# Optimization experiments

Hardware: AMD Instinct MI355X
Metric: run time of the kernel (lower is better)

Reference implementation:

```python
import jax, jax.numpy as jnp
import numpy as np

N_NODES = 50000
N_EDGES = 600000
IN_FEATS = 128
N_HIDDEN = 128
N_CLASSES = 40


def setup_inputs() -> dict:
    key = jax.random.key(0)
    ks = jax.random.split(key, 12)
    feat = jax.random.normal(ks[0], (N_NODES, IN_FEATS), dtype=jnp.float32)
    src = jax.random.randint(ks[1], (N_EDGES,), 0, N_NODES, dtype=jnp.int32)
    dst = jax.random.randint(ks[2], (N_EDGES,), 0, N_NODES, dtype=jnp.int32)
    dims = [(IN_FEATS, N_HIDDEN), (N_HIDDEN, N_HIDDEN), (N_HIDDEN, N_CLASSES)]
    params = {}
    for i, (di, do) in enumerate(dims):
        s = 1.0 / np.sqrt(di)
        params[f"w_self{i}"] = jax.random.uniform(ks[3 + 3 * i], (di, do), jnp.float32, -s, s)
        params[f"w_neigh{i}"] = jax.random.uniform(ks[4 + 3 * i], (di, do), jnp.float32, -s, s)
        params[f"b{i}"] = jnp.zeros((do,), jnp.float32)
    return dict(feat=feat, src=src, dst=dst, **params)


def _sage_layer(h, src, dst, w_self, w_neigh, b):
    # mean aggregation over in-neighbors: msg = h[src], reduce at dst
    msg_sum = jax.ops.segment_sum(h[src], dst, num_segments=N_NODES)  # [N, d]
    deg = jax.ops.segment_sum(jnp.ones((src.shape[0],), h.dtype), dst, num_segments=N_NODES)
    h_neigh = msg_sum / jnp.maximum(deg, 1.0)[:, None]
    # DGL SAGEConv(mean): out = fc_self(h) + fc_neigh(mean_neigh) + bias
    return h @ w_self + h_neigh @ w_neigh + b


def reference(feat, src, dst,
              w_self0, w_neigh0, b0,
              w_self1, w_neigh1, b1,
              w_self2, w_neigh2, b2):
    # dropout p=0.0 -> identity
    h = _sage_layer(feat, src, dst, w_self0, w_neigh0, b0)
    h = jax.nn.relu(h)
    h = _sage_layer(h, src, dst, w_self1, w_neigh1, b1)
    h = jax.nn.relu(h)
    h = _sage_layer(h, src, dst, w_self2, w_neigh2, b2)
    return h
```

## Files before the change

kernel.cpp:

```cpp
#include <hip/hip_runtime.h>

#define N_NODES 50000
#define N_EDGES 600000

typedef short bf16x8 __attribute__((ext_vector_type(8)));
typedef float f32x4  __attribute__((ext_vector_type(4)));
typedef unsigned short u16x8 __attribute__((ext_vector_type(8)));
typedef unsigned short u16x4 __attribute__((ext_vector_type(4)));

__device__ inline ushort rne_bf16(float a) {
    union { float f; unsigned u; } v; v.f = a;
    return (ushort)((v.u + 0x7FFFu + ((v.u >> 16) & 1u)) >> 16);
}
__device__ inline float bf16_to_f32(ushort h) {
    return __uint_as_float((unsigned)h << 16);
}
__device__ inline void split_bf16(float a, ushort& hi, ushort& lo) {
    hi = rne_bf16(a);
    float hv = bf16_to_f32(hi);
    lo = rne_bf16(a - hv);
}


__global__ void count_deg_kernel(const int* __restrict__ dst, int* __restrict__ deg, int ne) {
    int e = blockIdx.x * blockDim.x + threadIdx.x;
    if (e < ne) atomicAdd(&deg[dst[e]], 1);
}

__global__ __launch_bounds__(256) void block_sums_kernel(const int* __restrict__ deg,
                                                         int* __restrict__ bsum, int n) {
    __shared__ int s[256];
    int t = threadIdx.x;
    int i = blockIdx.x * 256 + t;
    s[t] = (i < n) ? deg[i] : 0;
    __syncthreads();
    #pragma unroll
    for (int d = 128; d > 0; d >>= 1) {
        if (t < d) s[t] += s[t + d];
        __syncthreads();
    }
    if (t == 0) bsum[blockIdx.x] = s[0];
}

__global__ __launch_bounds__(256) void scan_bsums_kernel(const int* __restrict__ bsum,
                                                         int* __restrict__ base, int nb,
                                                         int* __restrict__ off, int n) {
    __shared__ int s[256];
    int t = threadIdx.x;
    int v = (t < nb) ? bsum[t] : 0;
    s[t] = v;
    __syncthreads();
    #pragma unroll
    for (int d = 1; d < 256; d <<= 1) {
        int x = (t >= d) ? s[t - d] : 0;
        __syncthreads();
        s[t] += x;
        __syncthreads();
    }
    if (t < nb) base[t] = s[t] - v;
    if (t == 255) off[n] = s[255];
}

__global__ __launch_bounds__(256) void scatter_offsets_kernel(const int* __restrict__ deg,
                                                              const int* __restrict__ base,
                                                              int* __restrict__ off,
                                                              int* __restrict__ cur, int n) {
    __shared__ int s[256];
    int t = threadIdx.x;
    int i = blockIdx.x * 256 + t;
    int v = (i < n) ? deg[i] : 0;
    s[t] = v;
    __syncthreads();
    #pragma unroll
    for (int d = 1; d < 256; d <<= 1) {
        int x = (t >= d) ? s[t - d] : 0;
        __syncthreads();
        s[t] += x;
        __syncthreads();
    }
    if (i < n) {
        int excl = s[t] - v + base[blockIdx.x];
        off[i] = excl;
        cur[i] = excl;
    }
}

__global__ void fill_csr_kernel(const int* __restrict__ src, const int* __restrict__ dst,
                                int* __restrict__ cur, int* __restrict__ ssrc, int ne) {
    int e = blockIdx.x * blockDim.x + threadIdx.x;
    if (e < ne) {
        int p = atomicAdd(&cur[dst[e]], 1);
        ssrc[p] = src[e];
    }
}

__global__ void convert_w_kernel(const float* __restrict__ Ws, const float* __restrict__ Wn,
                                 int dout, ushort* __restrict__ Bth, ushort* __restrict__ Btl) {
    int n = blockIdx.x;
    int k = threadIdx.x;
    float w = (n < dout) ? Ws[(long)k * dout + n] : Wn[(long)k * dout + (n - dout)];
    ushort hi, lo;
    split_bf16(w, hi, lo);
    Bth[n * 128 + k] = hi;
    Btl[n * 128 + k] = lo;
}


#define KDIM 128
#define APAD 136

__device__ inline void stage_a_full(const float* __restrict__ A, int bm, int M, int tid,
                                    ushort* __restrict__ Ahi, ushort* __restrict__ Alo) {
    const int m  = tid >> 2;
    const int kq = (tid & 3) * 32;
    const int grow = bm + m;
    #pragma unroll
    for (int g = 0; g < 4; ++g) {
        float f[8];
        if (grow < M) {
            const float* ap = A + (long)grow * KDIM + kq + g * 8;
            float4 a0 = *(const float4*)ap;
            float4 a1 = *(const float4*)(ap + 4);
            f[0] = a0.x; f[1] = a0.y; f[2] = a0.z; f[3] = a0.w;
            f[4] = a1.x; f[5] = a1.y; f[6] = a1.z; f[7] = a1.w;
        } else {
            #pragma unroll
            for (int i = 0; i < 8; ++i) f[i] = 0.f;
        }
        ushort h[8], l[8];
        #pragma unroll
        for (int i = 0; i < 8; ++i) split_bf16(f[i], h[i], l[i]);
        uint4 hw, lw;
        hw.x = (unsigned)h[0] | ((unsigned)h[1] << 16);
        hw.y = (unsigned)h[2] | ((unsigned)h[3] << 16);
        hw.z = (unsigned)h[4] | ((unsigned)h[5] << 16);
        hw.w = (unsigned)h[6] | ((unsigned)h[7] << 16);
        lw.x = (unsigned)l[0] | ((unsigned)l[1] << 16);
        lw.y = (unsigned)l[2] | ((unsigned)l[3] << 16);
        lw.z = (unsigned)l[4] | ((unsigned)l[5] << 16);
        lw.w = (unsigned)l[6] | ((unsigned)l[7] << 16);
        *(uint4*)&Ahi[m * APAD + kq + g * 8] = hw;
        *(uint4*)&Alo[m * APAD + kq + g * 8] = lw;
    }
}

__global__ __launch_bounds__(256) void gemm_mfma_wide(
    const float* __restrict__ A,
    const ushort* __restrict__ Bth, const ushort* __restrict__ Btl,
    const float* __restrict__ bias,
    float* __restrict__ S, ushort* __restrict__ T, int M)
{
    __shared__ ushort Ahi[64 * APAD];
    __shared__ ushort Alo[64 * APAD];

    const int tid = threadIdx.x;
    const int wave = tid >> 6;
    const int lane = tid & 63;
    const int lane16 = lane & 15;
    const int quad = lane >> 4;
    const int bm = blockIdx.x * 64;
    const int colbase = wave * 64;

    stage_a_full(A, bm, M, tid, Ahi, Alo);
    __syncthreads();

    f32x4 acc[4][4] = {};

    #pragma unroll
    for (int c = 0; c < 4; ++c) {
        const int k0 = c * 32 + quad * 8;
        bf16x8 ah[4], al[4];
        #pragma unroll
        for (int r = 0; r < 4; ++r) {
            int off = (16 * r + lane16) * APAD + k0;
            ah[r] = *(const bf16x8*)&Ahi[off];
            al[r] = *(const bf16x8*)&Alo[off];
        }
        #pragma unroll
        for (int ct = 0; ct < 4; ++ct) {
            const long boff = (long)(colbase + 16 * ct + lane16) * KDIM + k0;
            bf16x8 bh = *(const bf16x8*)(Bth + boff);
            bf16x8 bl = *(const bf16x8*)(Btl + boff);
            #pragma unroll
            for (int r = 0; r < 4; ++r) {
                acc[r][ct] = __builtin_amdgcn_mfma_f32_16x16x32_bf16(bh, ah[r], acc[r][ct], 0, 0, 0);
                acc[r][ct] = __builtin_amdgcn_mfma_f32_16x16x32_bf16(bl, ah[r], acc[r][ct], 0, 0, 0);
                acc[r][ct] = __builtin_amdgcn_mfma_f32_16x16x32_bf16(bh, al[r], acc[r][ct], 0, 0, 0);
            }
        }
    }

    #pragma unroll
    for (int ct = 0; ct < 4; ++ct) {
        const int col0 = colbase + 16 * ct + quad * 4;
        const bool toS = col0 < 128;
        f32x4 bv = {0,0,0,0};
        if (toS) bv = *(const f32x4*)(bias + col0);
        #pragma unroll
        for (int r = 0; r < 4; ++r) {
            const int row = bm + 16 * r + lane16;
            if (row < M) {
                if (toS) {
                    *(f32x4*)(S + (long)row * 128 + col0) = acc[r][ct] + bv;
                } else {
                    u16x4 t4;
                    #pragma unroll
                    for (int i = 0; i < 4; ++i) t4[i] = rne_bf16(acc[r][ct][i]);
                    *(u16x4*)(T + (long)row * 128 + (col0 - 128)) = t4;
                }
            }
        }
    }
}

__global__ __launch_bounds__(256) void gemm_mfma_narrow(
    const float* __restrict__ A,
    const ushort* __restrict__ Bth, const ushort* __restrict__ Btl,
    const float* __restrict__ bias,
    float* __restrict__ S, ushort* __restrict__ T, int M)
{
    __shared__ ushort Ahi[64 * APAD];
    __shared__ ushort Alo[64 * APAD];

    const int tid = threadIdx.x;
    const int wave = tid >> 6;
    const int lane = tid & 63;
    const int lane16 = lane & 15;
    const int quad = lane >> 4;
    const int bm = blockIdx.x * 64;

    stage_a_full(A, bm, M, tid, Ahi, Alo);
    __syncthreads();

    f32x4 acc[5] = {};

    #pragma unroll
    for (int c = 0; c < 4; ++c) {
        const int k0 = c * 32 + quad * 8;
        const int off = (16 * wave + lane16) * APAD + k0;
        bf16x8 ah = *(const bf16x8*)&Ahi[off];
        bf16x8 al = *(const bf16x8*)&Alo[off];
        #pragma unroll
        for (int ct = 0; ct < 5; ++ct) {
            const long boff = (long)(16 * ct + lane16) * KDIM + k0;
            bf16x8 bh = *(const bf16x8*)(Bth + boff);
            bf16x8 bl = *(const bf16x8*)(Btl + boff);
            acc[ct] = __builtin_amdgcn_mfma_f32_16x16x32_bf16(bh, ah, acc[ct], 0, 0, 0);
            acc[ct] = __builtin_amdgcn_mfma_f32_16x16x32_bf16(bl, ah, acc[ct], 0, 0, 0);
            acc[ct] = __builtin_amdgcn_mfma_f32_16x16x32_bf16(bh, al, acc[ct], 0, 0, 0);
        }
    }

    #pragma unroll
    for (int ct = 0; ct < 5; ++ct) {
        const int col0 = 16 * ct + quad * 4;
        const bool toS = col0 < 40;
        const int row = bm + 16 * wave + lane16;
        if (row < M) {
            if (toS) {
                f32x4 bv = *(const f32x4*)(bias + col0);
                *(f32x4*)(S + (long)row * 40 + col0) = acc[ct] + bv;
            } else {
                u16x4 t4;
                #pragma unroll
                for (int i = 0; i < 4; ++i) t4[i] = rne_bf16(acc[ct][i]);
                *(u16x4*)(T + (long)row * 40 + (col0 - 40)) = t4;
            }
        }
    }
}


template <int RELU>
__global__ __launch_bounds__(256) void agg128_kernel(
    const float* __restrict__ S, const ushort* __restrict__ T,
    const int* __restrict__ off, const int* __restrict__ ssrc,
    float* __restrict__ out, int nnodes)
{
    const int node = (blockIdx.x * 256 + threadIdx.x) >> 6;
    if (node >= nnodes) return;
    const int lane = threadIdx.x & 63;
    const int slot = lane >> 4;
    const int col8 = (lane & 15) * 8;

    const int a = off[node];
    const int b = off[node + 1];

    f32x4 acc0a = {0,0,0,0}, acc0b = {0,0,0,0};
    f32x4 acc1a = {0,0,0,0}, acc1b = {0,0,0,0};

    int i = a;
    for (; i + 8 <= b; i += 8) {
        int s0 = ssrc[i + slot];
        int s1 = ssrc[i + 4 + slot];
        u16x8 v0 = *(const u16x8*)(T + (long)s0 * 128 + col8);
        u16x8 v1 = *(const u16x8*)(T + (long)s1 * 128 + col8);
        #pragma unroll
        for (int j = 0; j < 4; ++j) {
            acc0a[j] += bf16_to_f32(v0[j]);
            acc0b[j] += bf16_to_f32(v0[4 + j]);
            acc1a[j] += bf16_to_f32(v1[j]);
            acc1b[j] += bf16_to_f32(v1[4 + j]);
        }
    }
    for (; i < b; i += 4) {
        int e = i + slot;
        if (e < b) {
            int s = ssrc[e];
            u16x8 v = *(const u16x8*)(T + (long)s * 128 + col8);
            #pragma unroll
            for (int j = 0; j < 4; ++j) {
                acc0a[j] += bf16_to_f32(v[j]);
                acc0b[j] += bf16_to_f32(v[4 + j]);
            }
        }
    }
    f32x4 accA = acc0a + acc1a;
    f32x4 accB = acc0b + acc1b;

    #pragma unroll
    for (int m = 16; m <= 32; m <<= 1) {
        #pragma unroll
        for (int j = 0; j < 4; ++j) {
            accA[j] += __shfl_xor((float)accA[j], m);
            accB[j] += __shfl_xor((float)accB[j], m);
        }
    }

    if (slot == 0) {
        int deg = b - a;
        float scale = (deg > 0) ? (1.0f / (float)deg) : 0.f;
        f32x4 sA = *(const f32x4*)(S + (long)node * 128 + col8);
        f32x4 sB = *(const f32x4*)(S + (long)node * 128 + col8 + 4);
        f32x4 rA = sA + accA * scale;
        f32x4 rB = sB + accB * scale;
        if (RELU) {
            #pragma unroll
            for (int j = 0; j < 4; ++j) {
                rA[j] = fmaxf(rA[j], 0.f);
                rB[j] = fmaxf(rB[j], 0.f);
            }
        }
        *(f32x4*)(out + (long)node * 128 + col8) = rA;
        *(f32x4*)(out + (long)node * 128 + col8 + 4) = rB;
    }
}

template <int RELU>
__global__ __launch_bounds__(256) void agg40_kernel(
    const float* __restrict__ S, const ushort* __restrict__ T,
    const int* __restrict__ off, const int* __restrict__ ssrc,
    float* __restrict__ out, int nnodes)
{
    const int node = (blockIdx.x * 256 + threadIdx.x) >> 6;
    if (node >= nnodes) return;
    const int lane = threadIdx.x & 63;
    const bool active = lane < 60;
    const int slot = active ? (lane / 10) : 5;
    const int fi = lane % 10;
    const int fo = fi * 4;

    const int a = off[node];
    const int b = off[node + 1];

    f32x4 acc0 = {0,0,0,0}, acc1 = {0,0,0,0};

    int i = a;
    for (; i + 12 <= b; i += 12) {
        int s0 = ssrc[i + slot];
        int s1 = ssrc[i + 6 + slot];
        u16x4 v0 = *(const u16x4*)(T + (long)s0 * 40 + fo);
        u16x4 v1 = *(const u16x4*)(T + (long)s1 * 40 + fo);
        if (active) {
            #pragma unroll
            for (int j = 0; j < 4; ++j) {
                acc0[j] += bf16_to_f32(v0[j]);
                acc1[j] += bf16_to_f32(v1[j]);
            }
        }
    }
    for (; i < b; i += 6) {
        int e = i + slot;
        if (active && e < b) {
            int s = ssrc[e];
            u16x4 v = *(const u16x4*)(T + (long)s * 40 + fo);
            #pragma unroll
            for (int j = 0; j < 4; ++j) acc0[j] += bf16_to_f32(v[j]);
        }
    }
    f32x4 acc = acc0 + acc1;

    f32x4 tot = acc;
    #pragma unroll
    for (int d = 10; d <= 50; d += 10) {
        int srcl = fi + d;
        #pragma unroll
        for (int j = 0; j < 4; ++j) tot[j] += __shfl((float)acc[j], srcl);
    }

    if (lane < 10) {
        int deg = b - a;
        float scale = (deg > 0) ? (1.0f / (float)deg) : 0.f;
        f32x4 s4 = *(const f32x4*)(S + (long)node * 40 + fo);
        f32x4 r = s4 + tot * scale;
        if (RELU) {
            #pragma unroll
            for (int j = 0; j < 4; ++j) r[j] = fmaxf(r[j], 0.f);
        }
        *(f32x4*)(out + (long)node * 40 + fo) = r;
    }
}


extern "C" void kernel_launch(void* const* d_in, const int* in_sizes, int n_in,
                              void* d_out, int out_size, void* d_ws, size_t ws_size,
                              hipStream_t stream) {
    const float* feat = (const float*)d_in[0];
    const int*   src  = (const int*)d_in[1];
    const int*   dst  = (const int*)d_in[2];
    const float* ws0  = (const float*)d_in[3];
    const float* wn0  = (const float*)d_in[4];
    const float* b0   = (const float*)d_in[5];
    const float* ws1  = (const float*)d_in[6];
    const float* wn1  = (const float*)d_in[7];
    const float* b1   = (const float*)d_in[8];
    const float* ws2  = (const float*)d_in[9];
    const float* wn2  = (const float*)d_in[10];
    const float* b2   = (const float*)d_in[11];

    const int N = N_NODES;
    const int NE = N_EDGES;
    const int NB = (N + 255) / 256;

    char* ws = (char*)d_ws;
    int*    offsets = (int*)(ws + 0);
    int*    cursor  = (int*)(ws + 200704);
    int*    degi    = (int*)(ws + 401408);
    int*    bsum    = (int*)(ws + 601600);
    int*    bbase   = (int*)(ws + 602432);
    int*    ssrc    = (int*)(ws + 603648);
    ushort* Bth0 = (ushort*)(ws + 200704);
    ushort* Btl0 = (ushort*)(ws + 266240);
    ushort* Bth1 = (ushort*)(ws + 331776);
    ushort* Btl1 = (ushort*)(ws + 397312);
    ushort* Bth2 = (ushort*)(ws + 462848);
    ushort* Btl2 = (ushort*)(ws + 483328);
    float*  hbuf = (float*)(ws + 3003904);
    float*  sbuf = (float*)(ws + 28603904);
    ushort* tbuf = (ushort*)(ws + 54203904);

    hipMemsetAsync(degi, 0, (size_t)N * sizeof(int), stream);
    count_deg_kernel<<<(NE + 255) / 256, 256, 0, stream>>>(dst, degi, NE);
    block_sums_kernel<<<NB, 256, 0, stream>>>(degi, bsum, N);
    scan_bsums_kernel<<<1, 256, 0, stream>>>(bsum, bbase, NB, offsets, N);
    scatter_offsets_kernel<<<NB, 256, 0, stream>>>(degi, bbase, offsets, cursor, N);
    fill_csr_kernel<<<(NE + 255) / 256, 256, 0, stream>>>(src, dst, cursor, ssrc, NE);

    convert_w_kernel<<<256, 128, 0, stream>>>(ws0, wn0, 128, Bth0, Btl0);
    convert_w_kernel<<<256, 128, 0, stream>>>(ws1, wn1, 128, Bth1, Btl1);
    convert_w_kernel<<<80, 128, 0, stream>>>(ws2, wn2, 40, Bth2, Btl2);

    const int gx = (N + 63) / 64;
    const int ga = (N + 3) / 4;

    gemm_mfma_wide<<<gx, 256, 0, stream>>>(feat, Bth0, Btl0, b0, sbuf, tbuf, N);
    agg128_kernel<1><<<ga, 256, 0, stream>>>(sbuf, tbuf, offsets, ssrc, hbuf, N);

    gemm_mfma_wide<<<gx, 256, 0, stream>>>(hbuf, Bth1, Btl1, b1, sbuf, tbuf, N);
    agg128_kernel<1><<<ga, 256, 0, stream>>>(sbuf, tbuf, offsets, ssrc, hbuf, N);

    gemm_mfma_narrow<<<gx, 256, 0, stream>>>(hbuf, Bth2, Btl2, b2, sbuf, tbuf, N);
    agg40_kernel<0><<<ga, 256, 0, stream>>>(sbuf, tbuf, offsets, ssrc, (float*)d_out, N);
}
```

Measured before the change: 340.3 us.

## Fuse scan kernels, merge weight conversion launches, software-pipeline B loads in GEMMs

Merges the block-sum scan into the offset scatter kernel, with every block redundantly scanning the block sums, and merges the three weight-conversion launches into one. This cuts the launch count by three. The two MFMA GEMM kernels are restructured into a flattened loop that prefetches B fragments three iterations ahead through a small register ring, and gain launch_bounds occupancy hints. The prefetching adds register pressure, and the min-blocks hint could force spills.

```diff
diff --git a/kernel.cpp b/kernel.cpp
--- a/kernel.cpp
+++ b/kernel.cpp
@@ -42,13 +42,16 @@
     if (t == 0) bsum[blockIdx.x] = s[0];
 }
 
-__global__ __launch_bounds__(256) void scan_bsums_kernel(const int* __restrict__ bsum,
-                                                         int* __restrict__ base, int nb,
-                                                         int* __restrict__ off, int n) {
+__global__ __launch_bounds__(256) void scatter_fused_kernel(const int* __restrict__ deg,
+                                                            const int* __restrict__ bsum,
+                                                            int* __restrict__ off,
+                                                            int* __restrict__ cur,
+                                                            int n, int nb) {
     __shared__ int s[256];
     int t = threadIdx.x;
-    int v = (t < nb) ? bsum[t] : 0;
-    s[t] = v;
+
+    int bv = (t < nb) ? bsum[t] : 0;
+    s[t] = bv;
     __syncthreads();
     #pragma unroll
     for (int d = 1; d < 256; d <<= 1) {
@@ -57,16 +60,10 @@
         s[t] += x;
         __syncthreads();
     }
-    if (t < nb) base[t] = s[t] - v;
-    if (t == 255) off[n] = s[255];
-}
-
-__global__ __launch_bounds__(256) void scatter_offsets_kernel(const int* __restrict__ deg,
-                                                              const int* __restrict__ base,
-                                                              int* __restrict__ off,
-                                                              int* __restrict__ cur, int n) {
-    __shared__ int s[256];
-    int t = threadIdx.x;
+    int base = (blockIdx.x > 0) ? s[blockIdx.x - 1] : 0;
+    if (blockIdx.x == 0 && t == 0) off[n] = s[255];
+    __syncthreads();
+
     int i = blockIdx.x * 256 + t;
     int v = (i < n) ? deg[i] : 0;
     s[t] = v;
@@ -79,7 +76,7 @@
         __syncthreads();
     }
     if (i < n) {
-        int excl = s[t] - v + base[blockIdx.x];
+        int excl = s[t] - v + base;
         off[i] = excl;
         cur[i] = excl;
     }
@@ -94,15 +91,25 @@
     }
 }
 
-__global__ void convert_w_kernel(const float* __restrict__ Ws, const float* __restrict__ Wn,
-                                 int dout, ushort* __restrict__ Bth, ushort* __restrict__ Btl) {
-    int n = blockIdx.x;
+__global__ void convert_all_w(const float* __restrict__ ws0, const float* __restrict__ wn0,
+                              const float* __restrict__ ws1, const float* __restrict__ wn1,
+                              const float* __restrict__ ws2, const float* __restrict__ wn2,
+                              ushort* __restrict__ Bth0, ushort* __restrict__ Btl0,
+                              ushort* __restrict__ Bth1, ushort* __restrict__ Btl1,
+                              ushort* __restrict__ Bth2, ushort* __restrict__ Btl2) {
+    int b = blockIdx.x;
     int k = threadIdx.x;
+    const float *Ws, *Wn;
+    ushort *H, *L;
+    int dout, n;
+    if (b < 256)      { n = b;       dout = 128; Ws = ws0; Wn = wn0; H = Bth0; L = Btl0; }
+    else if (b < 512) { n = b - 256; dout = 128; Ws = ws1; Wn = wn1; H = Bth1; L = Btl1; }
+    else              { n = b - 512; dout = 40;  Ws = ws2; Wn = wn2; H = Bth2; L = Btl2; }
     float w = (n < dout) ? Ws[(long)k * dout + n] : Wn[(long)k * dout + (n - dout)];
     ushort hi, lo;
     split_bf16(w, hi, lo);
-    Bth[n * 128 + k] = hi;
-    Btl[n * 128 + k] = lo;
+    H[n * 128 + k] = hi;
+    L[n * 128 + k] = lo;
 }
 
 
@@ -144,7 +151,7 @@
     }
 }
 
-__global__ __launch_bounds__(256) void gemm_mfma_wide(
+__global__ __launch_bounds__(256, 3) void gemm_mfma_wide(
     const float* __restrict__ A,
     const ushort* __restrict__ Bth, const ushort* __restrict__ Btl,
     const float* __restrict__ bias,
@@ -164,29 +171,45 @@
     stage_a_full(A, bm, M, tid, Ahi, Alo);
     __syncthreads();
 
+    const ushort* Bh0 = Bth + (long)(colbase + lane16) * KDIM + quad * 8;
+    const ushort* Bl0 = Btl + (long)(colbase + lane16) * KDIM + quad * 8;
+
     f32x4 acc[4][4] = {};
-
-    #pragma unroll
-    for (int c = 0; c < 4; ++c) {
-        const int k0 = c * 32 + quad * 8;
-        bf16x8 ah[4], al[4];
+    bf16x8 bhb[4], blb[4];
+
+    #pragma unroll
+    for (int p = 0; p < 3; ++p) {
+        const int pc = p >> 2, pct = p & 3;
+        bhb[p] = *(const bf16x8*)(Bh0 + pct * 16 * KDIM + pc * 32);
+        blb[p] = *(const bf16x8*)(Bl0 + pct * 16 * KDIM + pc * 32);
+    }
+
+    bf16x8 ah[4], al[4];
+    #pragma unroll
+    for (int it = 0; it < 16; ++it) {
+        const int c = it >> 2, ct = it & 3;
+        if ((it & 3) == 0) {
+            const int k0 = c * 32 + quad * 8;
+            #pragma unroll
+            for (int r = 0; r < 4; ++r) {
+                int off = (16 * r + lane16) * APAD + k0;
+                ah[r] = *(const bf16x8*)&Ahi[off];
+                al[r] = *(const bf16x8*)&Alo[off];
+            }
+        }
+        const int nx = it + 3;
+        if (nx < 16) {
+            const int nc = nx >> 2, nct = nx & 3;
+            bhb[nx & 3] = *(const bf16x8*)(Bh0 + nct * 16 * KDIM + nc * 32);
+            blb[nx & 3] = *(const bf16x8*)(Bl0 + nct * 16 * KDIM + nc * 32);
+        }
+        const bf16x8 bh = bhb[it & 3];
+        const bf16x8 bl = blb[it & 3];
         #pragma unroll
         for (int r = 0; r < 4; ++r) {
-            int off = (16 * r + lane16) * APAD + k0;
-            ah[r] = *(const bf16x8*)&Ahi[off];
-            al[r] = *(const bf16x8*)&Alo[off];
-        }
-        #pragma unroll
-        for (int ct = 0; ct < 4; ++ct) {
-            const long boff = (long)(colbase + 16 * ct + lane16) * KDIM + k0;
-            bf16x8 bh = *(const bf16x8*)(Bth + boff);
-            bf16x8 bl = *(const bf16x8*)(Btl + boff);
-            #pragma unroll
-            for (int r = 0; r < 4; ++r) {
-                acc[r][ct] = __builtin_amdgcn_mfma_f32_16x16x32_bf16(bh, ah[r], acc[r][ct], 0, 0, 0);
-                acc[r][ct] = __builtin_amdgcn_mfma_f32_16x16x32_bf16(bl, ah[r], acc[r][ct], 0, 0, 0);
-                acc[r][ct] = __builtin_amdgcn_mfma_f32_16x16x32_bf16(bh, al[r], acc[r][ct], 0, 0, 0);
-            }
+            acc[r][ct] = __builtin_amdgcn_mfma_f32_16x16x32_bf16(bh, ah[r], acc[r][ct], 0, 0, 0);
+            acc[r][ct] = __builtin_amdgcn_mfma_f32_16x16x32_bf16(bl, ah[r], acc[r][ct], 0, 0, 0);
+            acc[r][ct] = __builtin_amdgcn_mfma_f32_16x16x32_bf16(bh, al[r], acc[r][ct], 0, 0, 0);
         }
     }
 
@@ -213,7 +236,7 @@
     }
 }
 
-__global__ __launch_bounds__(256) void gemm_mfma_narrow(
+__global__ __launch_bounds__(256, 3) void gemm_mfma_narrow(
     const float* __restrict__ A,
     const ushort* __restrict__ Bth, const ushort* __restrict__ Btl,
     const float* __restrict__ bias,
@@ -232,23 +255,39 @@
     stage_a_full(A, bm, M, tid, Ahi, Alo);
     __syncthreads();
 
+    const ushort* Bh0 = Bth + (long)lane16 * KDIM + quad * 8;
+    const ushort* Bl0 = Btl + (long)lane16 * KDIM + quad * 8;
+
     f32x4 acc[5] = {};
-
-    #pragma unroll
-    for (int c = 0; c < 4; ++c) {
-        const int k0 = c * 32 + quad * 8;
-        const int off = (16 * wave + lane16) * APAD + k0;
-        bf16x8 ah = *(const bf16x8*)&Ahi[off];
-        bf16x8 al = *(const bf16x8*)&Alo[off];
-        #pragma unroll
-        for (int ct = 0; ct < 5; ++ct) {
-            const long boff = (long)(16 * ct + lane16) * KDIM + k0;
-            bf16x8 bh = *(const bf16x8*)(Bth + boff);
-            bf16x8 bl = *(const bf16x8*)(Btl + boff);
-            acc[ct] = __builtin_amdgcn_mfma_f32_16x16x32_bf16(bh, ah, acc[ct], 0, 0, 0);
-            acc[ct] = __builtin_amdgcn_mfma_f32_16x16x32_bf16(bl, ah, acc[ct], 0, 0, 0);
-            acc[ct] = __builtin_amdgcn_mfma_f32_16x16x32_bf16(bh, al, acc[ct], 0, 0, 0);
-        }
+    bf16x8 bhb[4], blb[4];
+
+    #pragma unroll
+    for (int p = 0; p < 3; ++p) {
+        const int pc = p / 5, pct = p % 5;
+        bhb[p] = *(const bf16x8*)(Bh0 + pct * 16 * KDIM + pc * 32);
+        blb[p] = *(const bf16x8*)(Bl0 + pct * 16 * KDIM + pc * 32);
+    }
+
+    bf16x8 ah = {}, al = {};
+    #pragma unroll
+    for (int it = 0; it < 20; ++it) {
+        const int c = it / 5, ct = it % 5;
+        if (ct == 0) {
+            const int off = (16 * wave + lane16) * APAD + c * 32 + quad * 8;
+            ah = *(const bf16x8*)&Ahi[off];
+            al = *(const bf16x8*)&Alo[off];
+        }
+        const int nx = it + 3;
+        if (nx < 20) {
+            const int nc = nx / 5, nct = nx % 5;
+            bhb[nx & 3] = *(const bf16x8*)(Bh0 + nct * 16 * KDIM + nc * 32);
+            blb[nx & 3] = *(const bf16x8*)(Bl0 + nct * 16 * KDIM + nc * 32);
+        }
+        const bf16x8 bh = bhb[it & 3];
+        const bf16x8 bl = blb[it & 3];
+        acc[ct] = __builtin_amdgcn_mfma_f32_16x16x32_bf16(bh, ah, acc[ct], 0, 0, 0);
+        acc[ct] = __builtin_amdgcn_mfma_f32_16x16x32_bf16(bl, ah, acc[ct], 0, 0, 0);
+        acc[ct] = __builtin_amdgcn_mfma_f32_16x16x32_bf16(bh, al, acc[ct], 0, 0, 0);
     }
 
     #pragma unroll
@@ -437,7 +476,6 @@
     int*    cursor  = (int*)(ws + 200704);
     int*    degi    = (int*)(ws + 401408);
     int*    bsum    = (int*)(ws + 601600);
-    int*    bbase   = (int*)(ws + 602432);
     int*    ssrc    = (int*)(ws + 603648);
     ushort* Bth0 = (ushort*)(ws + 200704);
     ushort* Btl0 = (ushort*)(ws + 266240);
@@ -452,13 +490,11 @@
     hipMemsetAsync(degi, 0, (size_t)N * sizeof(int), stream);
     count_deg_kernel<<<(NE + 255) / 256, 256, 0, stream>>>(dst, degi, NE);
     block_sums_kernel<<<NB, 256, 0, stream>>>(degi, bsum, N);
-    scan_bsums_kernel<<<1, 256, 0, stream>>>(bsum, bbase, NB, offsets, N);
-    scatter_offsets_kernel<<<NB, 256, 0, stream>>>(degi, bbase, offsets, cursor, N);
+    scatter_fused_kernel<<<NB, 256, 0, stream>>>(degi, bsum, offsets, cursor, N, NB);
     fill_csr_kernel<<<(NE + 255) / 256, 256, 0, stream>>>(src, dst, cursor, ssrc, NE);
 
-    convert_w_kernel<<<256, 128, 0, stream>>>(ws0, wn0, 128, Bth0, Btl0);
-    convert_w_kernel<<<256, 128, 0, stream>>>(ws1, wn1, 128, Bth1, Btl1);
-    convert_w_kernel<<<80, 128, 0, stream>>>(ws2, wn2, 40, Bth2, Btl2);
+    convert_all_w<<<592, 128, 0, stream>>>(ws0, wn0, ws1, wn1, ws2, wn2,
+                                           Bth0, Btl0, Bth1, Btl1, Bth2, Btl2);
 
     const int gx = (N + 63) / 64;
     const int ga = (N + 3) / 4;
```

After: 330.4 us. 2.9% less time.
